# Kernel optimization log

Hardware: AMD Instinct MI355X
Metric: run time of the kernel (lower is better)

The kernel has to match this reference:

```python
import jax, jax.numpy as jnp
import numpy as np

ANCHORS = np.array([[10,13],[16,30],[33,23],[30,61],[62,45],[59,119],[116,90],[156,198],[373,326]], dtype=np.float32)
ANCHOR_MASK = [[6,7,8],[3,4,5],[0,1,2]]
CLASS_NUM = 80
IGNORE_THRESH = 0.5


def _bce_mean(z, x):
    # Keras BinaryCrossentropy(from_logits=True) called as a loss object:
    # elementwise sigmoid-CE, mean over last axis, then SUM_OVER_BATCH_SIZE
    # reduction == mean over ALL elements -> scalar.
    ce = jnp.maximum(x, 0.0) - x * z + jnp.log1p(jnp.exp(-jnp.abs(x)))
    return jnp.mean(ce)


def _layer_loss(out, lab, anchors):
    B, gh, gw, _ = out.shape
    A = anchors.shape[0]
    feats = out.reshape(B, gh, gw, A, CLASS_NUM + 5)
    anchors = jnp.asarray(anchors, dtype=jnp.float32)  # [A,2] (w,h)
    inp_wh = jnp.array([gw * 32, gh * 32], dtype=jnp.float32)  # reverse(input_shape)
    grid_wh = jnp.array([gw, gh], dtype=jnp.float32)           # reverse(grid_shape)

    gy, gx = jnp.meshgrid(jnp.arange(gh), jnp.arange(gw), indexing='ij')
    grid = jnp.stack([gx, gy], axis=-1).astype(jnp.float32)[:, :, None, :]  # [gh,gw,1,2]

    pred_xy = (jax.nn.sigmoid(feats[..., 0:2]) + grid) / grid_wh
    pred_wh = jnp.exp(feats[..., 2:4]) * anchors / inp_wh
    pred_box = jnp.concatenate([pred_xy, pred_wh], axis=-1)  # [B,gh,gw,A,4]

    obj = lab[..., 4:5]          # [B,gh,gw,A,1]
    objb = obj != 0.0
    N = gh * gw * A

    def _per_image(args):
        pb, tb, valid = args  # pb: [N,4] predicted, tb: [N,4] label boxes, valid: [N] bool
        b1_xy, b1_wh = pb[:, None, 0:2], pb[:, None, 2:4]
        b2_xy, b2_wh = tb[None, :, 0:2], tb[None, :, 2:4]
        b1_mins, b1_maxes = b1_xy - b1_wh / 2.0, b1_xy + b1_wh / 2.0
        b2_mins, b2_maxes = b2_xy - b2_wh / 2.0, b2_xy + b2_wh / 2.0
        inter_mins = jnp.maximum(b1_mins, b2_mins)
        inter_maxes = jnp.maximum(b1_maxes, b2_maxes)  # faithful to source (uses maximum, not minimum)
        inter_wh = jnp.maximum(inter_maxes - inter_mins, 0.0)
        inter = inter_wh[..., 0] * inter_wh[..., 1]
        a1 = b1_wh[..., 0] * b1_wh[..., 1]
        a2 = b2_wh[..., 0] * b2_wh[..., 1]
        iou = inter / (a1 + a2 - inter)  # [N,N]
        # only true boxes count; empty set -> best=-1 (matches tf reduce_max of empty = -inf)
        iou = jnp.where(valid[None, :], iou, -1.0)
        best_iou = jnp.max(iou, axis=-1)
        return (best_iou < IGNORE_THRESH).astype(jnp.float32)

    ignore = jax.lax.map(_per_image, (pred_box.reshape(B, N, 4),
                                      lab[..., 0:4].reshape(B, N, 4),
                                      objb.reshape(B, N)))
    ignore = jax.lax.stop_gradient(ignore).reshape(B, gh, gw, A, 1)

    raw_true_xy = lab[..., 0:2] * grid_wh - grid
    raw_true_wh = jnp.log(lab[..., 2:4] * inp_wh / anchors)
    raw_true_wh = jnp.where(objb, raw_true_wh, 0.0)
    box_loss_scale = 2.0 - lab[..., 2:3] * lab[..., 3:4]

    bf = jnp.float32(B)
    xy_loss = jnp.sum(obj * box_loss_scale * _bce_mean(raw_true_xy, feats[..., 0:2])) / bf
    wh_loss = jnp.sum(obj * box_loss_scale * 0.5 * jnp.square(raw_true_wh - feats[..., 2:4])) / bf
    conf_bce = _bce_mean(obj, feats[..., 4:5])
    conf_loss = jnp.sum(obj * conf_bce + (1.0 - obj) * conf_bce * ignore) / bf
    class_loss = jnp.sum(obj * _bce_mean(lab[..., 5:], feats[..., 5:])) / bf
    return xy_loss + wh_loss + conf_loss + class_loss


def _make_labels(key, B, g):
    k1, k2, k3, k4 = jax.random.split(key, 4)
    xy = jax.random.uniform(k1, (B, g, g, 3, 2), dtype=jnp.float32)
    wh = jax.random.uniform(k2, (B, g, g, 3, 2), dtype=jnp.float32, minval=0.05, maxval=1.0)
    objness = (jax.random.uniform(k3, (B, g, g, 3, 1)) < 0.02).astype(jnp.float32)
    cls = (jax.random.uniform(k4, (B, g, g, 3, CLASS_NUM)) < 0.05).astype(jnp.float32)
    return jnp.concatenate([xy, wh, objness, cls], axis=-1)


def setup_inputs() -> dict:
    key = jax.random.key(0)
    ks = jax.random.split(key, 6)
    B = 8
    grids = [13, 26, 52]
    out = {}
    for i, g in enumerate(grids):
        out[f'o{i}'] = jax.random.normal(ks[i], (B, g, g, 3 * (CLASS_NUM + 5)), dtype=jnp.float32)
        out[f'l{i}'] = _make_labels(ks[3 + i], B, g)
    return out


def reference(o0, o1, o2, l0, l1, l2):
    outputs = (o0, o1, o2)
    labels = (l0, l1, l2)
    loss = jnp.float32(0.0)
    for l in range(3):
        loss = loss + _layer_loss(outputs[l], labels[l], ANCHORS[ANCHOR_MASK[l]])
    return loss
```

## Files before the change

### kernel.cpp

```cpp
#include <hip/hip_runtime.h>
#include <math.h>

#define BDIM 256

__device__ __constant__ float c_aw[3][3] = {{116.f,156.f,373.f},{30.f,62.f,59.f},{10.f,16.f,33.f}};
__device__ __constant__ float c_ah[3][3] = {{90.f,198.f,326.f},{61.f,45.f,119.f},{13.f,30.f,23.f}};


__device__ __forceinline__ float bce_fast(float z, float x) {
    float t = __expf(-fabsf(x));
    return fmaxf(x, 0.f) - x * z + __logf(1.f + t);
}
__device__ __forceinline__ float bce4(const float4& z, const float4& x) {
    return bce_fast(z.x, x.x) + bce_fast(z.y, x.y)
         + bce_fast(z.z, x.z) + bce_fast(z.w, x.w);
}

__global__ __launch_bounds__(BDIM) void mega_a(
    const float* __restrict__ o0, const float* __restrict__ l0,
    const float* __restrict__ o1, const float* __restrict__ l1,
    const float* __restrict__ o2, const float* __restrict__ l2,
    double* __restrict__ acc, int* __restrict__ cnt, float4* __restrict__ tbox,
    float4* __restrict__ pbox, float* __restrict__ noobj)
{
    if (blockIdx.x < 1764) {
        int layer, blk0, nblk, n8;
        const float4 *O4, *L4;
        if (blockIdx.x < 84)       { layer=0; blk0=0;   nblk=84;   n8=43095;  O4=(const float4*)o0; L4=(const float4*)l0; }
        else if (blockIdx.x < 420) { layer=1; blk0=84;  nblk=336;  n8=172380; O4=(const float4*)o1; L4=(const float4*)l1; }
        else                       { layer=2; blk0=420; nblk=1344; n8=689520; O4=(const float4*)o2; L4=(const float4*)l2; }

        float s0 = 0.f, s1 = 0.f;
        for (int i = (int)(blockIdx.x - blk0) * BDIM + (int)threadIdx.x; i < n8;
             i += nblk * BDIM) {
            float4 a0 = O4[2*i], a1 = O4[2*i+1];
            float4 b0 = L4[2*i], b1 = L4[2*i+1];
            s0 += bce4(b0, a0);
            s1 += bce4(b1, a1);
        }
        float s = s0 + s1;
        __shared__ float sb[4];
        #pragma unroll
        for (int off = 32; off > 0; off >>= 1) s += __shfl_down(s, off, 64);
        if ((threadIdx.x & 63) == 0) sb[threadIdx.x >> 6] = s;
        __syncthreads();
        if (threadIdx.x == 0) {
            double t = (double)sb[0] + (double)sb[1] + (double)sb[2] + (double)sb[3];
            atomicAdd(&acc[layer * 8 + 0], t);
        }
        return;
    }

    int cb = blockIdx.x - 1764;
    int layer, blk0;
    if (cb < 16)      { layer = 0; blk0 = 0; }
    else if (cb < 80) { layer = 1; blk0 = 16; }
    else              { layer = 2; blk0 = 80; }
    const int g     = (layer == 0) ? 13 : (layer == 1) ? 26 : 52;
    const int Nlimg = g * g * 3;
    const int Cl    = 8 * Nlimg;
    const int cbase = (layer == 0) ? 0 : (layer == 1) ? 4056 : 20280;
    const float* O  = (layer == 0) ? o0 : (layer == 1) ? o1 : o2;
    const float* L  = (layer == 0) ? l0 : (layer == 1) ? l1 : l2;
    const float gf  = (float)g;
    const float inp = gf * 32.f;

    int cell = (cb - blk0) * BDIM + (int)threadIdx.x;
    float s_sub=0.f, s_xy=0.f, s_wh=0.f, s_conf=0.f, s_obj=0.f, s_s1=0.f;
    if (cell < Cl) {
        const float* op = O + (size_t)cell * 85;
        const float* lp = L + (size_t)cell * 85;
        float x0=op[0], x1=op[1], x2=op[2], x3=op[3], x4=op[4];
        float lx=lp[0], ly=lp[1], lw=lp[2], lh=lp[3], lobj=lp[4];
        int a  = cell % 3;
        int xi = (cell / 3) % g;
        int yi = (cell / (3 * g)) % g;
        int b  = cell / Nlimg;
        float aw = c_aw[layer][a], ah = c_ah[layer][a];

        float c4 = bce_fast(lobj, x4);
        s_sub  = bce_fast(lx,x0) + bce_fast(ly,x1)
               + bce_fast(lw,x2) + bce_fast(lh,x3) + c4;
        s_conf = c4;
        s_obj  = lobj;
        s_xy   = bce_fast(lx*gf - (float)xi, x0) + bce_fast(ly*gf - (float)yi, x1);

        float px = (1.f/(1.f+expf(-x0)) + (float)xi) / gf;
        float py = (1.f/(1.f+expf(-x1)) + (float)yi) / gf;
        float pw = expf(x2) * aw / inp;
        float ph = expf(x3) * ah / inp;
        pbox[cbase + cell]  = make_float4(px, py, pw, ph);
        noobj[cbase + cell] = 1.f - lobj;

        if (lobj != 0.f) {
            float bls = 2.f - lw * lh;
            s_s1 = lobj * bls;
            float dw = logf(lw * inp / aw) - x2;
            float dh = logf(lh * inp / ah) - x3;
            s_wh = lobj * bls * 0.5f * (dw * dw + dh * dh);
            int idx = atomicAdd(&cnt[layer * 8 + b], 1);
            tbox[cbase + b * Nlimg + idx] = make_float4(lx, ly, lw, lh);
        }
    }

    __shared__ float sb6[6][4];
    float v[6] = {s_sub, s_xy, s_wh, s_conf, s_obj, s_s1};
    #pragma unroll
    for (int q = 0; q < 6; q++) {
        float x = v[q];
        #pragma unroll
        for (int off = 32; off > 0; off >>= 1) x += __shfl_down(x, off, 64);
        if ((threadIdx.x & 63) == 0) sb6[q][threadIdx.x >> 6] = x;
    }
    __syncthreads();
    if (threadIdx.x < 6) {
        int q = threadIdx.x;
        double t = (double)sb6[q][0] + (double)sb6[q][1]
                 + (double)sb6[q][2] + (double)sb6[q][3];
        atomicAdd(&acc[layer * 8 + 1 + q], t);
    }
}

#define TCAP 512
#define NB_IGNORE 336
__global__ __launch_bounds__(BDIM) void ignore_fin(
    double* __restrict__ acc, const int* __restrict__ cnt,
    const float4* __restrict__ tbox, const float4* __restrict__ pbox,
    const float* __restrict__ noobj, int* __restrict__ done,
    float* __restrict__ out)
{
    int layer, img, chunk;
    if (blockIdx.x < 16)      { layer = 0; img = blockIdx.x >> 1; chunk = blockIdx.x & 1; }
    else if (blockIdx.x < 80) { int t = blockIdx.x - 16; layer = 1; img = t >> 3; chunk = t & 7; }
    else                      { int t = blockIdx.x - 80; layer = 2; img = t >> 5; chunk = t & 31; }
    const int g     = (layer == 0) ? 13 : (layer == 1) ? 26 : 52;
    const int Nlimg = g * g * 3;
    const int cbase = (layer == 0) ? 0 : (layer == 1) ? 4056 : 20280;

    int ci = chunk * BDIM + (int)threadIdx.x;
    bool live = (ci < Nlimg);
    int cell = cbase + img * Nlimg + (live ? ci : 0);

    float pminx=0, pmaxx=0, pminy=0, pmaxy=0, a1=0, nb=0;
    if (live) {
        float4 p = pbox[cell];
        pminx = p.x - p.z*0.5f; pmaxx = p.x + p.z*0.5f;
        pminy = p.y - p.w*0.5f; pmaxy = p.y + p.w*0.5f;
        a1 = p.z * p.w;
        nb = noobj[cell];
    }
    int n = cnt[layer * 8 + img];
    const float4* tp = tbox + cbase + img * Nlimg;

    __shared__ float4 sT[TCAP];
    float best = -1.f;
    bool donef = !live;
    for (int t0 = 0; t0 < n; t0 += TCAP) {
        int tn = min(TCAP, n - t0);
        __syncthreads();
        for (int i = threadIdx.x; i < tn; i += BDIM) sT[i] = tp[t0 + i];
        __syncthreads();
        if (!donef) {
            for (int j = 0; j < tn; j++) {
                float4 t = sT[j];
                float hw = t.z*0.5f, hh = t.w*0.5f;
                float imnx = fmaxf(pminx, t.x - hw);
                float imxx = fmaxf(pmaxx, t.x + hw);
                float imny = fmaxf(pminy, t.y - hh);
                float imxy = fmaxf(pmaxy, t.y + hh);
                float iw = fmaxf(imxx - imnx, 0.f);
                float ih = fmaxf(imxy - imny, 0.f);
                float inter = iw * ih;
                float iou = inter / (a1 + t.z*t.w - inter);
                best = fmaxf(best, iou);
                if (best >= 0.5f) { donef = true; break; }
            }
        }
    }
    float v = (live && best < 0.5f) ? nb : 0.f;

    __shared__ float sb[4];
    #pragma unroll
    for (int off = 32; off > 0; off >>= 1) v += __shfl_down(v, off, 64);
    if ((threadIdx.x & 63) == 0) sb[threadIdx.x >> 6] = v;
    __syncthreads();
    if (threadIdx.x == 0) {
        double t = (double)sb[0] + (double)sb[1] + (double)sb[2] + (double)sb[3];
        atomicAdd(&acc[layer * 8 + 7], t);
        __threadfence();
        int old = atomicAdd(done, 1);
        if (old == NB_IGNORE - 1) {
            __threadfence();
            double loss = 0.0;
            const int gs[3] = {13, 26, 52};
            for (int l = 0; l < 3; l++) {
                double C = 8.0 * gs[l] * gs[l] * 3.0;
                double q[8];
                #pragma unroll
                for (int k = 0; k < 8; k++)
                    q[k] = __hip_atomic_load(&acc[l*8+k], __ATOMIC_RELAXED,
                                             __HIP_MEMORY_SCOPE_AGENT);
                double cls = (q[0] - q[1]) / (C * 80.0);
                loss += ( (q[2]/(C*2.0))*q[6] + q[3]
                        + (q[4]/C)*(q[5]+q[7]) + cls*q[5] ) / 8.0;
            }
            out[0] = (float)loss;
        }
    }
}

extern "C" void kernel_launch(void* const* d_in, const int* in_sizes, int n_in,
                              void* d_out, int out_size, void* d_ws, size_t ws_size,
                              hipStream_t stream)
{
    const float* o0 = (const float*)d_in[0];
    const float* l0 = (const float*)d_in[1];
    const float* o1 = (const float*)d_in[2];
    const float* l1 = (const float*)d_in[3];
    const float* o2 = (const float*)d_in[4];
    const float* l2 = (const float*)d_in[5];

    double* acc   = (double*)d_ws;
    int*    cnt   = (int*)((char*)d_ws + 192);
    int*    done  = (int*)((char*)d_ws + 288);
    float4* tbox  = (float4*)((char*)d_ws + 512);
    float4* pbox  = (float4*)((char*)d_ws + 1363328);
    float*  noobj = (float*)((char*)d_ws + 2726144);

    hipMemsetAsync(d_ws, 0, 512, stream);
    mega_a<<<2098, BDIM, 0, stream>>>(o0, l0, o1, l1, o2, l2,
                                      acc, cnt, tbox, pbox, noobj);
    ignore_fin<<<NB_IGNORE, BDIM, 0, stream>>>(acc, cnt, tbox, pbox, noobj,
                                               done, (float*)d_out);
}
```

Before: 146.3 us.

## Fuse cell and ignore-IoU kernels via grid-wide spin gate in one launch

Merges the two kernels into one persistent launch. Cell blocks compute per-cell losses, publish true boxes with atomic stores, then spin on a global gate until every cell block has finished before running the ignore-IoU pass on predicted boxes still held in registers. This removes the second launch and the pbox/noobj round trip through global memory. The streaming BCE blocks are cut from 1764 to 626 and loop over more elements each. The spin-wait relies on all 334 cell blocks being co-resident, otherwise it deadlocks, and blocks spanning two images now loop over both.

```diff
diff --git a/kernel.cpp b/kernel.cpp
--- a/kernel.cpp
+++ b/kernel.cpp
@@ -2,6 +2,10 @@
 #include <math.h>
 
 #define BDIM 256
+#define NCELLB 334
+#define NSTREAMB 626
+#define NBLK (NCELLB + NSTREAMB)
+#define TCAP 512
 
 __device__ __constant__ float c_aw[3][3] = {{116.f,156.f,373.f},{30.f,62.f,59.f},{10.f,16.f,33.f}};
 __device__ __constant__ float c_ah[3][3] = {{90.f,198.f,326.f},{61.f,45.f,119.f},{13.f,30.f,23.f}};
@@ -16,180 +20,12 @@
          + bce_fast(z.z, x.z) + bce_fast(z.w, x.w);
 }
 
-__global__ __launch_bounds__(BDIM) void mega_a(
-    const float* __restrict__ o0, const float* __restrict__ l0,
-    const float* __restrict__ o1, const float* __restrict__ l1,
-    const float* __restrict__ o2, const float* __restrict__ l2,
-    double* __restrict__ acc, int* __restrict__ cnt, float4* __restrict__ tbox,
-    float4* __restrict__ pbox, float* __restrict__ noobj)
-{
-    if (blockIdx.x < 1764) {
-        int layer, blk0, nblk, n8;
-        const float4 *O4, *L4;
-        if (blockIdx.x < 84)       { layer=0; blk0=0;   nblk=84;   n8=43095;  O4=(const float4*)o0; L4=(const float4*)l0; }
-        else if (blockIdx.x < 420) { layer=1; blk0=84;  nblk=336;  n8=172380; O4=(const float4*)o1; L4=(const float4*)l1; }
-        else                       { layer=2; blk0=420; nblk=1344; n8=689520; O4=(const float4*)o2; L4=(const float4*)l2; }
-
-        float s0 = 0.f, s1 = 0.f;
-        for (int i = (int)(blockIdx.x - blk0) * BDIM + (int)threadIdx.x; i < n8;
-             i += nblk * BDIM) {
-            float4 a0 = O4[2*i], a1 = O4[2*i+1];
-            float4 b0 = L4[2*i], b1 = L4[2*i+1];
-            s0 += bce4(b0, a0);
-            s1 += bce4(b1, a1);
-        }
-        float s = s0 + s1;
-        __shared__ float sb[4];
-        #pragma unroll
-        for (int off = 32; off > 0; off >>= 1) s += __shfl_down(s, off, 64);
-        if ((threadIdx.x & 63) == 0) sb[threadIdx.x >> 6] = s;
-        __syncthreads();
-        if (threadIdx.x == 0) {
-            double t = (double)sb[0] + (double)sb[1] + (double)sb[2] + (double)sb[3];
-            atomicAdd(&acc[layer * 8 + 0], t);
-        }
-        return;
-    }
-
-    int cb = blockIdx.x - 1764;
-    int layer, blk0;
-    if (cb < 16)      { layer = 0; blk0 = 0; }
-    else if (cb < 80) { layer = 1; blk0 = 16; }
-    else              { layer = 2; blk0 = 80; }
-    const int g     = (layer == 0) ? 13 : (layer == 1) ? 26 : 52;
-    const int Nlimg = g * g * 3;
-    const int Cl    = 8 * Nlimg;
-    const int cbase = (layer == 0) ? 0 : (layer == 1) ? 4056 : 20280;
-    const float* O  = (layer == 0) ? o0 : (layer == 1) ? o1 : o2;
-    const float* L  = (layer == 0) ? l0 : (layer == 1) ? l1 : l2;
-    const float gf  = (float)g;
-    const float inp = gf * 32.f;
-
-    int cell = (cb - blk0) * BDIM + (int)threadIdx.x;
-    float s_sub=0.f, s_xy=0.f, s_wh=0.f, s_conf=0.f, s_obj=0.f, s_s1=0.f;
-    if (cell < Cl) {
-        const float* op = O + (size_t)cell * 85;
-        const float* lp = L + (size_t)cell * 85;
-        float x0=op[0], x1=op[1], x2=op[2], x3=op[3], x4=op[4];
-        float lx=lp[0], ly=lp[1], lw=lp[2], lh=lp[3], lobj=lp[4];
-        int a  = cell % 3;
-        int xi = (cell / 3) % g;
-        int yi = (cell / (3 * g)) % g;
-        int b  = cell / Nlimg;
-        float aw = c_aw[layer][a], ah = c_ah[layer][a];
-
-        float c4 = bce_fast(lobj, x4);
-        s_sub  = bce_fast(lx,x0) + bce_fast(ly,x1)
-               + bce_fast(lw,x2) + bce_fast(lh,x3) + c4;
-        s_conf = c4;
-        s_obj  = lobj;
-        s_xy   = bce_fast(lx*gf - (float)xi, x0) + bce_fast(ly*gf - (float)yi, x1);
-
-        float px = (1.f/(1.f+expf(-x0)) + (float)xi) / gf;
-        float py = (1.f/(1.f+expf(-x1)) + (float)yi) / gf;
-        float pw = expf(x2) * aw / inp;
-        float ph = expf(x3) * ah / inp;
-        pbox[cbase + cell]  = make_float4(px, py, pw, ph);
-        noobj[cbase + cell] = 1.f - lobj;
-
-        if (lobj != 0.f) {
-            float bls = 2.f - lw * lh;
-            s_s1 = lobj * bls;
-            float dw = logf(lw * inp / aw) - x2;
-            float dh = logf(lh * inp / ah) - x3;
-            s_wh = lobj * bls * 0.5f * (dw * dw + dh * dh);
-            int idx = atomicAdd(&cnt[layer * 8 + b], 1);
-            tbox[cbase + b * Nlimg + idx] = make_float4(lx, ly, lw, lh);
-        }
-    }
-
-    __shared__ float sb6[6][4];
-    float v[6] = {s_sub, s_xy, s_wh, s_conf, s_obj, s_s1};
-    #pragma unroll
-    for (int q = 0; q < 6; q++) {
-        float x = v[q];
-        #pragma unroll
-        for (int off = 32; off > 0; off >>= 1) x += __shfl_down(x, off, 64);
-        if ((threadIdx.x & 63) == 0) sb6[q][threadIdx.x >> 6] = x;
-    }
-    __syncthreads();
-    if (threadIdx.x < 6) {
-        int q = threadIdx.x;
-        double t = (double)sb6[q][0] + (double)sb6[q][1]
-                 + (double)sb6[q][2] + (double)sb6[q][3];
-        atomicAdd(&acc[layer * 8 + 1 + q], t);
-    }
-}
-
-#define TCAP 512
-#define NB_IGNORE 336
-__global__ __launch_bounds__(BDIM) void ignore_fin(
-    double* __restrict__ acc, const int* __restrict__ cnt,
-    const float4* __restrict__ tbox, const float4* __restrict__ pbox,
-    const float* __restrict__ noobj, int* __restrict__ done,
-    float* __restrict__ out)
-{
-    int layer, img, chunk;
-    if (blockIdx.x < 16)      { layer = 0; img = blockIdx.x >> 1; chunk = blockIdx.x & 1; }
-    else if (blockIdx.x < 80) { int t = blockIdx.x - 16; layer = 1; img = t >> 3; chunk = t & 7; }
-    else                      { int t = blockIdx.x - 80; layer = 2; img = t >> 5; chunk = t & 31; }
-    const int g     = (layer == 0) ? 13 : (layer == 1) ? 26 : 52;
-    const int Nlimg = g * g * 3;
-    const int cbase = (layer == 0) ? 0 : (layer == 1) ? 4056 : 20280;
-
-    int ci = chunk * BDIM + (int)threadIdx.x;
-    bool live = (ci < Nlimg);
-    int cell = cbase + img * Nlimg + (live ? ci : 0);
-
-    float pminx=0, pmaxx=0, pminy=0, pmaxy=0, a1=0, nb=0;
-    if (live) {
-        float4 p = pbox[cell];
-        pminx = p.x - p.z*0.5f; pmaxx = p.x + p.z*0.5f;
-        pminy = p.y - p.w*0.5f; pmaxy = p.y + p.w*0.5f;
-        a1 = p.z * p.w;
-        nb = noobj[cell];
-    }
-    int n = cnt[layer * 8 + img];
-    const float4* tp = tbox + cbase + img * Nlimg;
-
-    __shared__ float4 sT[TCAP];
-    float best = -1.f;
-    bool donef = !live;
-    for (int t0 = 0; t0 < n; t0 += TCAP) {
-        int tn = min(TCAP, n - t0);
-        __syncthreads();
-        for (int i = threadIdx.x; i < tn; i += BDIM) sT[i] = tp[t0 + i];
-        __syncthreads();
-        if (!donef) {
-            for (int j = 0; j < tn; j++) {
-                float4 t = sT[j];
-                float hw = t.z*0.5f, hh = t.w*0.5f;
-                float imnx = fmaxf(pminx, t.x - hw);
-                float imxx = fmaxf(pmaxx, t.x + hw);
-                float imny = fmaxf(pminy, t.y - hh);
-                float imxy = fmaxf(pmaxy, t.y + hh);
-                float iw = fmaxf(imxx - imnx, 0.f);
-                float ih = fmaxf(imxy - imny, 0.f);
-                float inter = iw * ih;
-                float iou = inter / (a1 + t.z*t.w - inter);
-                best = fmaxf(best, iou);
-                if (best >= 0.5f) { donef = true; break; }
-            }
-        }
-    }
-    float v = (live && best < 0.5f) ? nb : 0.f;
-
-    __shared__ float sb[4];
-    #pragma unroll
-    for (int off = 32; off > 0; off >>= 1) v += __shfl_down(v, off, 64);
-    if ((threadIdx.x & 63) == 0) sb[threadIdx.x >> 6] = v;
-    __syncthreads();
+__device__ __forceinline__ void block_done(double* acc, int* done, float* out) {
     if (threadIdx.x == 0) {
-        double t = (double)sb[0] + (double)sb[1] + (double)sb[2] + (double)sb[3];
-        atomicAdd(&acc[layer * 8 + 7], t);
         __threadfence();
-        int old = atomicAdd(done, 1);
-        if (old == NB_IGNORE - 1) {
+        int old = __hip_atomic_fetch_add(done, 1, __ATOMIC_ACQ_REL,
+                                         __HIP_MEMORY_SCOPE_AGENT);
+        if (old == NBLK - 1) {
             __threadfence();
             double loss = 0.0;
             const int gs[3] = {13, 26, 52};
@@ -209,6 +45,192 @@
     }
 }
 
+__global__ __launch_bounds__(BDIM, 4) void yolo_fused(
+    const float* __restrict__ o0, const float* __restrict__ l0,
+    const float* __restrict__ o1, const float* __restrict__ l1,
+    const float* __restrict__ o2, const float* __restrict__ l2,
+    double* __restrict__ acc, int* __restrict__ cnt, float4* __restrict__ tbox,
+    int* __restrict__ done, int* __restrict__ gate, float* __restrict__ out)
+{
+    if (blockIdx.x >= NCELLB) {
+        int sb = blockIdx.x - NCELLB;
+        int layer, blk0, nblk, n8;
+        const float4 *O4, *L4;
+        if (sb < 30)       { layer=0; blk0=0;   nblk=30;  n8=43095;  O4=(const float4*)o0; L4=(const float4*)l0; }
+        else if (sb < 149) { layer=1; blk0=30;  nblk=119; n8=172380; O4=(const float4*)o1; L4=(const float4*)l1; }
+        else               { layer=2; blk0=149; nblk=477; n8=689520; O4=(const float4*)o2; L4=(const float4*)l2; }
+
+        float s0 = 0.f, s1 = 0.f;
+        for (int i = (sb - blk0) * BDIM + (int)threadIdx.x; i < n8;
+             i += nblk * BDIM) {
+            float4 a0 = O4[2*i], a1 = O4[2*i+1];
+            float4 b0 = L4[2*i], b1 = L4[2*i+1];
+            s0 += bce4(b0, a0);
+            s1 += bce4(b1, a1);
+        }
+        float s = s0 + s1;
+        __shared__ float sbm[4];
+        #pragma unroll
+        for (int off = 32; off > 0; off >>= 1) s += __shfl_down(s, off, 64);
+        if ((threadIdx.x & 63) == 0) sbm[threadIdx.x >> 6] = s;
+        __syncthreads();
+        if (threadIdx.x == 0) {
+            double t = (double)sbm[0] + (double)sbm[1] + (double)sbm[2] + (double)sbm[3];
+            atomicAdd(&acc[layer * 8 + 0], t);
+        }
+        block_done(acc, done, out);
+        return;
+    }
+
+    int cb = blockIdx.x;
+    int layer, blk0;
+    if (cb < 16)      { layer = 0; blk0 = 0; }
+    else if (cb < 80) { layer = 1; blk0 = 16; }
+    else              { layer = 2; blk0 = 80; }
+    const int g     = (layer == 0) ? 13 : (layer == 1) ? 26 : 52;
+    const int Nlimg = g * g * 3;
+    const int Cl    = 8 * Nlimg;
+    const int cbase = (layer == 0) ? 0 : (layer == 1) ? 4056 : 20280;
+    const float* O  = (layer == 0) ? o0 : (layer == 1) ? o1 : o2;
+    const float* L  = (layer == 0) ? l0 : (layer == 1) ? l1 : l2;
+    const float gf  = (float)g;
+    const float inp = gf * 32.f;
+
+    int  cell = (cb - blk0) * BDIM + (int)threadIdx.x;
+    bool live = (cell < Cl);
+    float s_sub=0.f, s_xy=0.f, s_wh=0.f, s_conf=0.f, s_obj=0.f, s_s1=0.f;
+    float pminx=0.f, pmaxx=0.f, pminy=0.f, pmaxy=0.f, a1v=0.f, nbv=0.f;
+    int b = 0;
+    if (live) {
+        const float* op = O + (size_t)cell * 85;
+        const float* lp = L + (size_t)cell * 85;
+        float x0=op[0], x1=op[1], x2=op[2], x3=op[3], x4=op[4];
+        float lx=lp[0], ly=lp[1], lw=lp[2], lh=lp[3], lobj=lp[4];
+        int a  = cell % 3;
+        int xi = (cell / 3) % g;
+        int yi = (cell / (3 * g)) % g;
+        b      = cell / Nlimg;
+        float aw = c_aw[layer][a], ah = c_ah[layer][a];
+
+        float c4 = bce_fast(lobj, x4);
+        s_sub  = bce_fast(lx,x0) + bce_fast(ly,x1)
+               + bce_fast(lw,x2) + bce_fast(lh,x3) + c4;
+        s_conf = c4;
+        s_obj  = lobj;
+        s_xy   = bce_fast(lx*gf - (float)xi, x0) + bce_fast(ly*gf - (float)yi, x1);
+
+        float px = (1.f/(1.f+expf(-x0)) + (float)xi) / gf;
+        float py = (1.f/(1.f+expf(-x1)) + (float)yi) / gf;
+        float pw = expf(x2) * aw / inp;
+        float ph = expf(x3) * ah / inp;
+        pminx = px - pw*0.5f; pmaxx = px + pw*0.5f;
+        pminy = py - ph*0.5f; pmaxy = py + ph*0.5f;
+        a1v = pw * ph;
+        nbv = 1.f - lobj;
+
+        if (lobj != 0.f) {
+            float bls = 2.f - lw * lh;
+            s_s1 = lobj * bls;
+            float dw = logf(lw * inp / aw) - x2;
+            float dh = logf(lh * inp / ah) - x3;
+            s_wh = lobj * bls * 0.5f * (dw * dw + dh * dh);
+            int idx = atomicAdd(&cnt[layer * 8 + b], 1);
+            float* dst = (float*)&tbox[cbase + b * Nlimg + idx];
+            __hip_atomic_store(dst+0, lx, __ATOMIC_RELAXED, __HIP_MEMORY_SCOPE_AGENT);
+            __hip_atomic_store(dst+1, ly, __ATOMIC_RELAXED, __HIP_MEMORY_SCOPE_AGENT);
+            __hip_atomic_store(dst+2, lw, __ATOMIC_RELAXED, __HIP_MEMORY_SCOPE_AGENT);
+            __hip_atomic_store(dst+3, lh, __ATOMIC_RELAXED, __HIP_MEMORY_SCOPE_AGENT);
+        }
+    }
+
+    __shared__ float sb6[6][4];
+    {
+        float v[6] = {s_sub, s_xy, s_wh, s_conf, s_obj, s_s1};
+        #pragma unroll
+        for (int q = 0; q < 6; q++) {
+            float x = v[q];
+            #pragma unroll
+            for (int off = 32; off > 0; off >>= 1) x += __shfl_down(x, off, 64);
+            if ((threadIdx.x & 63) == 0) sb6[q][threadIdx.x >> 6] = x;
+        }
+        __syncthreads();
+        if (threadIdx.x < 6) {
+            int q = threadIdx.x;
+            double t = (double)sb6[q][0] + (double)sb6[q][1]
+                     + (double)sb6[q][2] + (double)sb6[q][3];
+            atomicAdd(&acc[layer * 8 + 1 + q], t);
+        }
+    }
+
+    __syncthreads();
+    if (threadIdx.x == 0) {
+        __threadfence();
+        __hip_atomic_fetch_add(gate, 1, __ATOMIC_ACQ_REL, __HIP_MEMORY_SCOPE_AGENT);
+        while (__hip_atomic_load(gate, __ATOMIC_ACQUIRE, __HIP_MEMORY_SCOPE_AGENT)
+               < NCELLB)
+            __builtin_amdgcn_s_sleep(2);
+        __threadfence();
+    }
+    __syncthreads();
+
+    int cellFirst = (cb - blk0) * BDIM;
+    int cellLast  = min(cellFirst + BDIM - 1, Cl - 1);
+    int imgA = cellFirst / Nlimg;
+    int imgB = cellLast  / Nlimg;
+
+    __shared__ float4 sT[TCAP];
+    float best = -1.f;
+    bool donef = !live;
+    for (int im = imgA; im <= imgB; ++im) {
+        int n = __hip_atomic_load(&cnt[layer*8+im], __ATOMIC_RELAXED,
+                                  __HIP_MEMORY_SCOPE_AGENT);
+        const float4* tp = tbox + cbase + im * Nlimg;
+        bool mine = live && (b == im);
+        for (int t0 = 0; t0 < n; t0 += TCAP) {
+            int tn = min(TCAP, n - t0);
+            __syncthreads();
+            for (int i = threadIdx.x; i < tn; i += BDIM) {
+                const float* s = (const float*)(tp + t0 + i);
+                float4 t;
+                t.x = __hip_atomic_load(s+0, __ATOMIC_RELAXED, __HIP_MEMORY_SCOPE_AGENT);
+                t.y = __hip_atomic_load(s+1, __ATOMIC_RELAXED, __HIP_MEMORY_SCOPE_AGENT);
+                t.z = __hip_atomic_load(s+2, __ATOMIC_RELAXED, __HIP_MEMORY_SCOPE_AGENT);
+                t.w = __hip_atomic_load(s+3, __ATOMIC_RELAXED, __HIP_MEMORY_SCOPE_AGENT);
+                sT[i] = t;
+            }
+            __syncthreads();
+            if (mine && !donef) {
+                for (int j = 0; j < tn; j++) {
+                    float4 t = sT[j];
+                    float hw = t.z*0.5f, hh = t.w*0.5f;
+                    float imnx = fmaxf(pminx, t.x - hw);
+                    float imxx = fmaxf(pmaxx, t.x + hw);
+                    float imny = fmaxf(pminy, t.y - hh);
+                    float imxy = fmaxf(pmaxy, t.y + hh);
+                    float iw = fmaxf(imxx - imnx, 0.f);
+                    float ih = fmaxf(imxy - imny, 0.f);
+                    float inter = iw * ih;
+                    float iou = inter / (a1v + t.z*t.w - inter);
+                    best = fmaxf(best, iou);
+                    if (best >= 0.5f) { donef = true; break; }
+                }
+            }
+        }
+    }
+    float v = (live && best < 0.5f) ? nbv : 0.f;
+
+    __shared__ float sbi[4];
+    #pragma unroll
+    for (int off = 32; off > 0; off >>= 1) v += __shfl_down(v, off, 64);
+    if ((threadIdx.x & 63) == 0) sbi[threadIdx.x >> 6] = v;
+    __syncthreads();
+    if (threadIdx.x == 0) {
+        double t = (double)sbi[0] + (double)sbi[1] + (double)sbi[2] + (double)sbi[3];
+        atomicAdd(&acc[layer * 8 + 7], t);
+    }
+    block_done(acc, done, out);
+}
+
 extern "C" void kernel_launch(void* const* d_in, const int* in_sizes, int n_in,
                               void* d_out, int out_size, void* d_ws, size_t ws_size,
                               hipStream_t stream)
@@ -220,16 +242,14 @@
     const float* o2 = (const float*)d_in[4];
     const float* l2 = (const float*)d_in[5];
 
-    double* acc   = (double*)d_ws;
-    int*    cnt   = (int*)((char*)d_ws + 192);
-    int*    done  = (int*)((char*)d_ws + 288);
-    float4* tbox  = (float4*)((char*)d_ws + 512);
-    float4* pbox  = (float4*)((char*)d_ws + 1363328);
-    float*  noobj = (float*)((char*)d_ws + 2726144);
+    double* acc  = (double*)d_ws;
+    int*    cnt  = (int*)((char*)d_ws + 192);
+    int*    done = (int*)((char*)d_ws + 288);
+    int*    gate = (int*)((char*)d_ws + 292);
+    float4* tbox = (float4*)((char*)d_ws + 512);
 
     hipMemsetAsync(d_ws, 0, 512, stream);
-    mega_a<<<2098, BDIM, 0, stream>>>(o0, l0, o1, l1, o2, l2,
-                                      acc, cnt, tbox, pbox, noobj);
-    ignore_fin<<<NB_IGNORE, BDIM, 0, stream>>>(acc, cnt, tbox, pbox, noobj,
-                                               done, (float*)d_out);
-}
+    yolo_fused<<<NBLK, BDIM, 0, stream>>>(o0, l0, o1, l1, o2, l2,
+                                          acc, cnt, tbox, done, gate,
+                                          (float*)d_out);
+}
```

Result: slower. 220.9 us (+51.0%).
